# Performance work log

Hardware: AMD Instinct MI355X
Metric: run time of the kernel (lower is better)

Reference implementation:

```python
import jax, jax.numpy as jnp
import numpy as np

B, Zc, Hin, Win = 256, 2048, 7, 7
S = 8            # SPATIAL_ : everything resized to 8x8
WIN = 2          # window_size
P = WIN * WIN    # 4 pixels per patch
N = (S // WIN) ** 2  # 16 patches
Q = 1            # ELM hidden neurons


def _lcg(m, n):
    """Deterministic LCG pseudo-random weights used by RADAM's RNN_AE."""
    L = m * n
    if L == 1:
        return np.ones((1, 1))
    V = np.zeros(L)
    V[0] = L + 1
    a, b, c = L + 2, L + 3, L * L
    for i in range(1, L):
        V[i] = (a * V[i - 1] + b) % c
    V = (V - V.mean()) / V.std()  # zscore (ddof=0, scipy default)
    return V.reshape(m, n)


def setup_inputs() -> dict:
    key = jax.random.key(0)
    x = jax.random.normal(key, (B, Zc, Hin, Win), dtype=jnp.float32)
    Wlcg = jnp.asarray(_lcg(Q, P + 1), dtype=jnp.float32)  # (Q, P+1) encoder weights incl. bias
    return {"x": x, "Wlcg": Wlcg}


def _zscore(a, axis):
    m = jnp.mean(a, axis=axis, keepdims=True)
    s = jnp.std(a, axis=axis, keepdims=True)  # ddof=0 like scipy.stats.zscore
    return jnp.nan_to_num((a - m) / s)


def reference(x, Wlcg):
    b, z = x.shape[:2]
    # torchvision Resize(8): bilinear resize to 8x8 (upsample here, antialias irrelevant)
    xr = jax.image.resize(x, (b, z, S, S), method="bilinear")
    # einops: 'b c (h p1) (w p2) -> b c (p1 p2) (h w)' with p1=p2=2
    g = S // WIN  # 4
    p = xr.reshape(b, z, g, WIN, g, WIN).transpose(0, 1, 3, 5, 2, 4).reshape(b, z, P, N)
    # stats.zscore over channel axis (axis=0 per sample) + nan_to_num
    p = _zscore(p, axis=1)
    # RNN_AE.fit: zscore each spectra over pixel axis (axis=0 of (P,N)) + nan_to_num
    Xc = _zscore(p, axis=2)                                   # (b, z, P, N)
    ones = jnp.ones((b, z, 1, N), Xc.dtype)
    Xb = jnp.concatenate([ones, Xc], axis=2)                  # (b, z, P+1, N) bias row
    hidden = jax.nn.sigmoid(jnp.einsum("qp,bzpn->bzqn", Wlcg, Xb))  # (b, z, Q, N)
    # closed-form AE decoder: beta = X Z^T (Z Z^T)^{-1}  (Q=1 -> scalar inverse)
    zz = jnp.sum(hidden * hidden, axis=-1, keepdims=True)     # (b, z, Q, 1)
    beta = jnp.einsum("bzpn,bzqn->bzpq", Xc, hidden) / jnp.swapaxes(zz, -1, -2)  # (b, z, P, Q)
    # std-pool decoder weights over pixel axis -> one scalar per channel
    feat = jnp.std(beta, axis=2)                              # (b, z, 1)
    return feat
```

## Files before the change

kernel.cpp:

```cpp
#include <hip/hip_runtime.h>
#include <math.h>

#define REC_LEN 49
#define NPOS 64

__device__ __forceinline__ void patchvals(const float* __restrict__ in, float* __restrict__ out) {
    const float wA[8] = {1.f, 0.1875f, 0.3125f, 0.4375f, 0.5625f, 0.6875f, 0.8125f, 1.f};
    const float wB[8] = {0.f, 0.8125f, 0.6875f, 0.5625f, 0.4375f, 0.3125f, 0.1875f, 0.f};
    const int  i0[8]  = {0, 0, 1, 2, 3, 4, 5, 6};
    const int  i1[8]  = {0, 1, 2, 3, 4, 5, 6, 6};
#pragma unroll
    for (int r = 0; r < 8; ++r) {
        float tmp[7];
#pragma unroll
        for (int c = 0; c < 7; ++c)
            tmp[c] = wA[r] * in[i0[r] * 7 + c] + wB[r] * in[i1[r] * 7 + c];
#pragma unroll
        for (int c = 0; c < 8; ++c) {
            float vv = wA[c] * tmp[i0[c]] + wB[c] * tmp[i1[c]];
            int k = (((r & 1) * 2 + (c & 1)) << 4) + ((r >> 1) << 2) + (c >> 1);
            out[k] = vv;
        }
    }
}

template<int W>
__device__ __forceinline__ void load_rec(const float* __restrict__ xblk, int lane, float* __restrict__ in) {
    const float4* p = (const float4*)xblk + 49 * lane + 12 * W;
    float4 f[13];
#pragma unroll
    for (int i = 0; i < 13; ++i) f[i] = p[i];
    const float* ff = (const float*)f;
#pragma unroll
    for (int j = 0; j < 49; ++j) in[j] = ff[W + j];
}

#define LOAD_REC_SWITCH(xblk, lane, in, w)            \
    switch (w) {                                      \
        case 0:  load_rec<0>(xblk, lane, in); break;  \
        case 1:  load_rec<1>(xblk, lane, in); break;  \
        case 2:  load_rec<2>(xblk, lane, in); break;  \
        default: load_rec<3>(xblk, lane, in); break;  \
    }

__device__ __forceinline__ void fold64(float* a, int lane) {
#pragma unroll
    for (int m = 32; m >= 1; m >>= 1) {
        const bool hi = (lane & m) != 0;
#pragma unroll
        for (int i = 0; i < m; ++i) {
            float x0 = a[i], x1 = a[i + m];
            float mine  = hi ? x1 : x0;
            float other = hi ? x0 : x1;
            a[i] = mine + __shfl_xor(other, m, 64);
        }
    }
}

extern "C" __global__ void __launch_bounds__(256)
k_stats(const float* __restrict__ x, float* __restrict__ part) {
    const int tid = threadIdx.x;
    const int lane = tid & 63, w = tid >> 6;
    const float* xblk = x + (size_t)blockIdx.x * (256 * REC_LEN);

    float in[REC_LEN];
    LOAD_REC_SWITCH(xblk, lane, in, w);

    float v[NPOS];
    patchvals(in, v);
    float sq[NPOS];
#pragma unroll
    for (int k = 0; k < NPOS; ++k) sq[k] = v[k] * v[k];

    fold64(v, lane);
    fold64(sq, lane);

    __shared__ float red[4][2][64];
    red[w][0][lane] = v[0];
    red[w][1][lane] = sq[0];
    __syncthreads();
    if (tid < 64) {
        float s  = red[0][0][tid] + red[1][0][tid] + red[2][0][tid] + red[3][0][tid];
        float s2 = red[0][1][tid] + red[1][1][tid] + red[2][1][tid] + red[3][1][tid];
        part[(size_t)blockIdx.x * 128 + tid]      = s;
        part[(size_t)blockIdx.x * 128 + 64 + tid] = s2;
    }
}

extern "C" __global__ void __launch_bounds__(256)
k_final(const float* __restrict__ x, const float* __restrict__ Wl,
        const float* __restrict__ part, float* __restrict__ out) {
    __shared__ float msh[NPOS], ish[NPOS];
    const int tid = threadIdx.x;
    const int lane = tid & 63, w = tid >> 6;
    const int b = blockIdx.x >> 3;
    const float* xblk = x + (size_t)blockIdx.x * (256 * REC_LEN);

    float in[REC_LEN];
    LOAD_REC_SWITCH(xblk, lane, in, w);

    if (tid < 64) {
        float s = 0.f, s2 = 0.f;
#pragma unroll
        for (int c = 0; c < 8; ++c) {
            const float* p = part + (size_t)(b * 8 + c) * 128;
            s  += p[tid];
            s2 += p[64 + tid];
        }
        float m   = s * (1.f / 2048.f);
        float var = fmaf(-m, m, s2 * (1.f / 2048.f));
        msh[tid] = m;
        ish[tid] = var > 0.f ? rsqrtf(var) : 0.f;
    }
    __syncthreads();

    float v[NPOS];
    patchvals(in, v);

#pragma unroll
    for (int k = 0; k < NPOS; ++k)
        v[k] = (v[k] - msh[k]) * ish[k];

    const float w0 = Wl[0], w1 = Wl[1], w2 = Wl[2], w3 = Wl[3], w4 = Wl[4];
    float zz = 0.f, sp0 = 0.f, sp1 = 0.f, sp2 = 0.f, sp3 = 0.f;
#pragma unroll
    for (int n = 0; n < 16; ++n) {
        float a0 = v[n], a1 = v[16 + n], a2 = v[32 + n], a3 = v[48 + n];
        float m4 = 0.25f * (a0 + a1 + a2 + a3);
        float d0 = a0 - m4, d1 = a1 - m4, d2 = a2 - m4, d3 = a3 - m4;
        float var4 = 0.25f * (d0 * d0 + d1 * d1 + d2 * d2 + d3 * d3);
        float inv4 = var4 > 0.f ? rsqrtf(var4) : 0.f;
        float x0 = d0 * inv4, x1 = d1 * inv4, x2 = d2 * inv4, x3 = d3 * inv4;
        float t = w0 + w1 * x0 + w2 * x1 + w3 * x2 + w4 * x3;
        float h = 1.f / (1.f + expf(-t));
        zz += h * h;
        sp0 += x0 * h; sp1 += x1 * h; sp2 += x2 * h; sp3 += x3 * h;
    }
    float izz = 1.f / zz;
    float b0 = sp0 * izz, b1 = sp1 * izz, b2 = sp2 * izz, b3 = sp3 * izz;
    float mb = 0.25f * (b0 + b1 + b2 + b3);
    float e0 = b0 - mb, e1 = b1 - mb, e2 = b2 - mb, e3 = b3 - mb;
    out[(size_t)blockIdx.x * 256 + 4 * lane + w] =
        sqrtf(0.25f * (e0 * e0 + e1 * e1 + e2 * e2 + e3 * e3));
}

extern "C" void kernel_launch(void* const* d_in, const int* in_sizes, int n_in,
                              void* d_out, int out_size, void* d_ws, size_t ws_size,
                              hipStream_t stream) {
    (void)in_sizes; (void)n_in; (void)out_size; (void)ws_size;
    const float* x  = (const float*)d_in[0];
    const float* Wl = (const float*)d_in[1];
    float* out  = (float*)d_out;
    float* part = (float*)d_ws;

    k_stats<<<2048, 256, 0, stream>>>(x, part);
    k_final<<<2048, 256, 0, stream>>>(x, Wl, part, out);
}
```

Baseline: 217.3 us.

## Use permlane swaps for reductions, fast math intrinsics, and occupancy hints

```diff
diff --git a/kernel.cpp b/kernel.cpp
--- a/kernel.cpp
+++ b/kernel.cpp
@@ -14,10 +14,12 @@
         float tmp[7];
 #pragma unroll
         for (int c = 0; c < 7; ++c)
-            tmp[c] = wA[r] * in[i0[r] * 7 + c] + wB[r] * in[i1[r] * 7 + c];
+            tmp[c] = (r == 0 || r == 7) ? in[i0[r] * 7 + c]
+                     : wA[r] * in[i0[r] * 7 + c] + wB[r] * in[i1[r] * 7 + c];
 #pragma unroll
         for (int c = 0; c < 8; ++c) {
-            float vv = wA[c] * tmp[i0[c]] + wB[c] * tmp[i1[c]];
+            float vv = (c == 0 || c == 7) ? tmp[i0[c]]
+                       : wA[c] * tmp[i0[c]] + wB[c] * tmp[i1[c]];
             int k = (((r & 1) * 2 + (c & 1)) << 4) + ((r >> 1) << 2) + (c >> 1);
             out[k] = vv;
         }
@@ -43,21 +45,16 @@
         default: load_rec<3>(xblk, lane, in); break;  \
     }
 
-__device__ __forceinline__ void fold64(float* a, int lane) {
-#pragma unroll
-    for (int m = 32; m >= 1; m >>= 1) {
-        const bool hi = (lane & m) != 0;
-#pragma unroll
-        for (int i = 0; i < m; ++i) {
-            float x0 = a[i], x1 = a[i + m];
-            float mine  = hi ? x1 : x0;
-            float other = hi ? x0 : x1;
-            a[i] = mine + __shfl_xor(other, m, 64);
-        }
-    }
+__device__ __forceinline__ float swap32_add(float a, float b) {
+    asm volatile("v_permlane32_swap_b32 %0, %1" : "+v"(a), "+v"(b));
+    return a + b;
+}
+__device__ __forceinline__ float swap16_add(float a, float b) {
+    asm volatile("v_permlane16_swap_b32 %0, %1" : "+v"(a), "+v"(b));
+    return a + b;
 }
 
-extern "C" __global__ void __launch_bounds__(256)
+extern "C" __global__ void __launch_bounds__(256, 3)
 k_stats(const float* __restrict__ x, float* __restrict__ part) {
     const int tid = threadIdx.x;
     const int lane = tid & 63, w = tid >> 6;
@@ -68,26 +65,46 @@
 
     float v[NPOS];
     patchvals(in, v);
-    float sq[NPOS];
+
+    float a[32], s[32];
 #pragma unroll
-    for (int k = 0; k < NPOS; ++k) sq[k] = v[k] * v[k];
-
-    fold64(v, lane);
-    fold64(sq, lane);
+    for (int i = 0; i < 32; ++i) {
+        float qa = v[i] * v[i], qb = v[i + 32] * v[i + 32];
+        a[i] = swap32_add(v[i], v[i + 32]);
+        s[i] = swap32_add(qa, qb);
+    }
+#pragma unroll
+    for (int i = 0; i < 16; ++i) {
+        a[i] = swap16_add(a[i], a[i + 16]);
+        s[i] = swap16_add(s[i], s[i + 16]);
+    }
+#pragma unroll
+    for (int m = 8; m >= 1; m >>= 1) {
+        const bool hi = (lane & m) != 0;
+#pragma unroll
+        for (int i = 0; i < m; ++i) {
+            float x0 = a[i], x1 = a[i + m];
+            float mine = hi ? x1 : x0, oth = hi ? x0 : x1;
+            a[i] = mine + __shfl_xor(oth, m);
+            float y0 = s[i], y1 = s[i + m];
+            float nine = hi ? y1 : y0, oth2 = hi ? y0 : y1;
+            s[i] = nine + __shfl_xor(oth2, m);
+        }
+    }
 
     __shared__ float red[4][2][64];
-    red[w][0][lane] = v[0];
-    red[w][1][lane] = sq[0];
+    red[w][0][lane] = a[0];
+    red[w][1][lane] = s[0];
     __syncthreads();
     if (tid < 64) {
-        float s  = red[0][0][tid] + red[1][0][tid] + red[2][0][tid] + red[3][0][tid];
-        float s2 = red[0][1][tid] + red[1][1][tid] + red[2][1][tid] + red[3][1][tid];
-        part[(size_t)blockIdx.x * 128 + tid]      = s;
-        part[(size_t)blockIdx.x * 128 + 64 + tid] = s2;
+        float S  = red[0][0][tid] + red[1][0][tid] + red[2][0][tid] + red[3][0][tid];
+        float S2 = red[0][1][tid] + red[1][1][tid] + red[2][1][tid] + red[3][1][tid];
+        part[(size_t)blockIdx.x * 128 + tid]      = S;
+        part[(size_t)blockIdx.x * 128 + 64 + tid] = S2;
     }
 }
 
-extern "C" __global__ void __launch_bounds__(256)
+extern "C" __global__ void __launch_bounds__(256, 3)
 k_final(const float* __restrict__ x, const float* __restrict__ Wl,
         const float* __restrict__ part, float* __restrict__ out) {
     __shared__ float msh[NPOS], ish[NPOS];
@@ -100,17 +117,17 @@
     LOAD_REC_SWITCH(xblk, lane, in, w);
 
     if (tid < 64) {
-        float s = 0.f, s2 = 0.f;
+        float S = 0.f, S2 = 0.f;
 #pragma unroll
         for (int c = 0; c < 8; ++c) {
             const float* p = part + (size_t)(b * 8 + c) * 128;
-            s  += p[tid];
-            s2 += p[64 + tid];
+            S  += p[tid];
+            S2 += p[64 + tid];
         }
-        float m   = s * (1.f / 2048.f);
-        float var = fmaf(-m, m, s2 * (1.f / 2048.f));
+        float m   = S * (1.f / 2048.f);
+        float var = fmaf(-m, m, S2 * (1.f / 2048.f));
         msh[tid] = m;
-        ish[tid] = var > 0.f ? rsqrtf(var) : 0.f;
+        ish[tid] = var > 0.f ? __builtin_amdgcn_rsqf(var) : 0.f;
     }
     __syncthreads();
 
@@ -129,14 +146,14 @@
         float m4 = 0.25f * (a0 + a1 + a2 + a3);
         float d0 = a0 - m4, d1 = a1 - m4, d2 = a2 - m4, d3 = a3 - m4;
         float var4 = 0.25f * (d0 * d0 + d1 * d1 + d2 * d2 + d3 * d3);
-        float inv4 = var4 > 0.f ? rsqrtf(var4) : 0.f;
+        float inv4 = var4 > 0.f ? __builtin_amdgcn_rsqf(var4) : 0.f;
         float x0 = d0 * inv4, x1 = d1 * inv4, x2 = d2 * inv4, x3 = d3 * inv4;
         float t = w0 + w1 * x0 + w2 * x1 + w3 * x2 + w4 * x3;
-        float h = 1.f / (1.f + expf(-t));
+        float h = __builtin_amdgcn_rcpf(1.f + __expf(-t));
         zz += h * h;
         sp0 += x0 * h; sp1 += x1 * h; sp2 += x2 * h; sp3 += x3 * h;
     }
-    float izz = 1.f / zz;
+    float izz = __builtin_amdgcn_rcpf(zz);
     float b0 = sp0 * izz, b1 = sp1 * izz, b2 = sp2 * izz, b3 = sp3 * izz;
     float mb = 0.25f * (b0 + b1 + b2 + b3);
     float e0 = b0 - mb, e1 = b1 - mb, e2 = b2 - mb, e3 = b3 - mb;
```

Result: slower. 234.4 us (+7.9%).
